# Kernel optimization log

Measured on AMD Instinct MI355X. Metric: run time of the kernel, lower is better.

## Reference

```python
import jax, jax.numpy as jnp
import numpy as np

NUM_USERS = 50000
NUM_ITEMS = 50000
U_IN = 256
I_IN = 256
LATENT = 128
FINAL = 64
NUM_U_GRAPHS = 2
NUM_I_GRAPHS = 2
E = 1000000
BATCH = 16384


def _seg_softmax(scores, seg, n):
    # numerically-stable segment softmax (PyG softmax semantics)
    m = jax.ops.segment_max(scores, seg, num_segments=n)
    e = jnp.exp(scores - m[seg])
    s = jax.ops.segment_sum(e, seg, num_segments=n)
    return e / (s[seg] + 1e-16)


def _gat(S, edges, W1, a_self, a_nb, omega):
    # S: [N, in_dim], edges: [G, 2, E] (row 0 = src j, row 1 = dst i)
    n = S.shape[0]
    H1 = S @ W1                     # [N, latent]
    alpha_self = H1 @ a_self        # [N]
    alpha_nb = H1 @ a_nb            # [N]
    H2 = jnp.zeros_like(H1)
    for g in range(edges.shape[0]):  # small fixed loop over graphs
        src = edges[g, 0]
        dst = edges[g, 1]
        score = jax.nn.leaky_relu(alpha_self[dst] + alpha_nb[src], negative_slope=0.2)
        alpha = _seg_softmax(score, dst, n)                      # [E]
        msg = H1[src] * alpha[:, None]                           # [E, latent]
        H2 = H2 + omega[g] * jax.ops.segment_sum(msg, dst, num_segments=n)
    return H2


def setup_inputs() -> dict:
    key = jax.random.key(0)
    ks = jax.random.split(key, 24)
    d = {}
    d['user_indices'] = jax.random.randint(ks[0], (BATCH,), 0, NUM_USERS)
    d['item_indices'] = jax.random.randint(ks[1], (BATCH,), 0, NUM_ITEMS)
    d['S_u'] = jax.random.normal(ks[2], (NUM_USERS, U_IN), dtype=jnp.float32)
    d['S_b'] = jax.random.normal(ks[3], (NUM_ITEMS, I_IN), dtype=jnp.float32)
    d['edges_u'] = jax.random.randint(ks[4], (NUM_U_GRAPHS, 2, E), 0, NUM_USERS)
    d['edges_b'] = jax.random.randint(ks[5], (NUM_I_GRAPHS, 2, E), 0, NUM_ITEMS)
    s = 0.05
    d['W1_u'] = jax.random.normal(ks[6], (U_IN, LATENT), dtype=jnp.float32) * s
    d['a_self_u'] = jax.random.normal(ks[7], (LATENT,), dtype=jnp.float32) * s
    d['a_nb_u'] = jax.random.normal(ks[8], (LATENT,), dtype=jnp.float32) * s
    d['omega_u'] = jnp.ones((NUM_U_GRAPHS,), dtype=jnp.float32)
    d['W1_b'] = jax.random.normal(ks[9], (I_IN, LATENT), dtype=jnp.float32) * s
    d['a_self_b'] = jax.random.normal(ks[10], (LATENT,), dtype=jnp.float32) * s
    d['a_nb_b'] = jax.random.normal(ks[11], (LATENT,), dtype=jnp.float32) * s
    d['omega_b'] = jnp.ones((NUM_I_GRAPHS,), dtype=jnp.float32)
    d['Wu2'] = jax.random.normal(ks[12], (LATENT, LATENT), dtype=jnp.float32) * s
    d['Wus2_w'] = jax.random.normal(ks[13], (U_IN, LATENT), dtype=jnp.float32) * s
    d['Wus2_b'] = jnp.zeros((LATENT,), dtype=jnp.float32)
    d['Wb2'] = jax.random.normal(ks[14], (LATENT, LATENT), dtype=jnp.float32) * s
    d['Wbs2_w'] = jax.random.normal(ks[15], (I_IN, LATENT), dtype=jnp.float32) * s
    d['Wbs2_b'] = jnp.zeros((LATENT,), dtype=jnp.float32)
    d['Wu3'] = jax.random.normal(ks[16], (LATENT, FINAL), dtype=jnp.float32) * s
    d['Wb3'] = jax.random.normal(ks[17], (LATENT, FINAL), dtype=jnp.float32) * s
    d['Hu4'] = jax.random.normal(ks[18], (NUM_USERS, FINAL), dtype=jnp.float32) * 0.01
    d['Hb4'] = jax.random.normal(ks[19], (NUM_ITEMS, FINAL), dtype=jnp.float32) * 0.01
    d['bu'] = jnp.zeros((NUM_USERS,), dtype=jnp.float32)
    d['bb'] = jnp.zeros((NUM_ITEMS,), dtype=jnp.float32)
    d['bx'] = jnp.zeros((), dtype=jnp.float32)
    return d


def reference(user_indices, item_indices, S_u, S_b, edges_u, edges_b,
              W1_u, a_self_u, a_nb_u, omega_u,
              W1_b, a_self_b, a_nb_b, omega_b,
              Wu2, Wus2_w, Wus2_b, Wb2, Wbs2_w, Wbs2_b,
              Wu3, Wb3, Hu4, Hb4, bu, bb, bx):
    r_min, r_max = 1.0, 5.0
    H_u_2 = _gat(S_u, edges_u, W1_u, a_self_u, a_nb_u, omega_u)
    H_b_2 = _gat(S_b, edges_b, W1_b, a_self_b, a_nb_b, omega_b)
    H_u_3 = jax.nn.elu(H_u_2 @ Wu2 + S_u @ Wus2_w + Wus2_b)
    H_b_3 = jax.nn.elu(H_b_2 @ Wb2 + S_b @ Wbs2_w + Wbs2_b)
    U_all = jax.nn.elu(H_u_3 @ Wu3) + Hu4
    B_all = jax.nn.elu(H_b_3 @ Wb3) + Hb4
    U_batch = U_all[user_indices]
    B_batch = B_all[item_indices]
    dot = jnp.sum(U_batch * B_batch, axis=1)
    raw = dot + bu[user_indices] + bb[item_indices] + bx
    return (r_max - r_min) * jax.nn.sigmoid(raw) + r_min
```

## Files before the change

### kernel.cpp

```cpp
#include <hip/hip_runtime.h>
#include <math.h>

#define N_NODES 50000
#define IN_DIM  256
#define LATENT  128
#define FINALD  64
#define NGRAPH  2
#define NEDGE   1000000
#define BATCHSZ 16384

#define VN4     (4 * N_NODES)
#define NBU     ((VN4 + 255) >> 8)
#define E4      (4 * NEDGE)
#define NPB     256
#define PCH     ((E4 + NPB - 1) / NPB)
#define BCAP    8192
#define PREPB   768

#define WSP_SIDE   98304
#define HSTRIDE    (N_NODES * LATENT)
#define H1STRIDE8  ((size_t)N_NODES * 128)

typedef __attribute__((ext_vector_type(8))) short bf16x8;
typedef __attribute__((ext_vector_type(8))) _Float16 f16x8;
typedef __attribute__((ext_vector_type(4))) float f32x4;
typedef __attribute__((ext_vector_type(2))) float f32x2;
typedef __attribute__((ext_vector_type(8))) unsigned short u16x8;
typedef __attribute__((ext_vector_type(2))) unsigned int u32x2;

__device__ inline unsigned short f2bf(float x) {
    unsigned int u = __float_as_uint(x);
    u = (u + 0x7fffu + ((u >> 16) & 1u)) >> 16;
    return (unsigned short)u;
}
__device__ inline float bf2f(unsigned short h) {
    return __uint_as_float(((unsigned int)h) << 16);
}
__device__ inline unsigned char f2fp8(float x) {
    int p = __builtin_amdgcn_cvt_pk_fp8_f32(x, x, 0, false);
    return (unsigned char)(p & 0xFF);
}

#define BM 128
#define BK 64

__device__ inline int swz(int r, int k) {
    return r * BK + ((((k >> 3) ^ (r & 7)) << 3) | (k & 7));
}
__device__ inline int swz2(int r, int c) {
    return r * 128 + ((((c >> 3) ^ (r & 7)) << 3) | (c & 7));
}

__device__ inline void edge_decomp(int i, int& side, int& g, int& idx) {
    if (i < NEDGE)          { side = 0; g = 0; idx = i; }
    else if (i < 2 * NEDGE) { side = 0; g = 1; idx = i - NEDGE; }
    else if (i < 3 * NEDGE) { side = 1; g = 0; idx = i - 2 * NEDGE; }
    else                    { side = 1; g = 1; idx = i - 3 * NEDGE; }
}

__global__ __launch_bounds__(256)
void fat_count_prep(const int* __restrict__ eU, const int* __restrict__ eB,
                    int* __restrict__ pcnt,
                    const float* __restrict__ W1u, const float* __restrict__ Wu2,
                    const float* __restrict__ Wus2, const float* __restrict__ Wu3,
                    const float* __restrict__ W1b, const float* __restrict__ Wb2,
                    const float* __restrict__ Wbs2, const float* __restrict__ Wb3,
                    unsigned short* __restrict__ dst)
{
    __shared__ int h[NBU];
    int tid = threadIdx.x;
    if (blockIdx.x < NPB) {
        for (int i = tid; i < NBU; i += 256) h[i] = 0;
        __syncthreads();
        int start = blockIdx.x * PCH;
        int stop  = min(start + PCH, E4);
        for (int i = start + tid; i < stop; i += 256) {
            int side, g, idx;
            edge_decomp(i, side, g, idx);
            const int* base = side ? eB : eU;
            int d = base[(size_t)(2 * g + 1) * NEDGE + idx];
            int vd = side * (2 * N_NODES) + g * N_NODES + d;
            atomicAdd(&h[vd >> 8], 1);
        }
        __syncthreads();
        for (int i = tid; i < NBU; i += 256)
            pcnt[i * NPB + blockIdx.x] = h[i];
    } else {
        int e = (blockIdx.x - NPB) * 256 + tid;
        if (e >= 2 * WSP_SIDE) return;
        int side = e >= WSP_SIDE;
        int r = e - (side ? WSP_SIDE : 0);
        const float* src; int K, hoff; int w3 = 0, fp16 = 0;
        if (r < 32768)      { src = side ? W1b  : W1u;  K = 256; hoff = 0;     }
        else if (r < 49152) { src = side ? Wb2  : Wu2;  K = 128; hoff = 32768; r -= 32768; fp16 = 1; }
        else if (r < 81920) { src = side ? Wbs2 : Wus2; K = 256; hoff = 49152; r -= 49152; }
        else                { src = side ? Wb3  : Wu3;  K = 128; hoff = 81920; r -= 81920; w3 = 1; }
        int n = (K == 256) ? (r >> 8) : (r >> 7);
        int k = (K == 256) ? (r & 255) : (r & 127);
        float x;
        if (w3) x = (n < 64) ? src[k * 64 + n] : 0.f;
        else    x = src[k * 128 + n];
        unsigned short o;
        if (fp16) { _Float16 hx = (_Float16)x; o = *(unsigned short*)&hx; }
        else      o = f2bf(x);
        dst[(size_t)side * WSP_SIDE + hoff + n * K + k] = o;
    }
}

__global__ __launch_bounds__(1024)
void part_scan(const int* __restrict__ pcnt, int* __restrict__ pbase,
               int* __restrict__ bbase, int* __restrict__ offs)
{
    __shared__ int btot[NBU];
    __shared__ int wsum2[16];
    int tid = threadIdx.x;
    int lane = tid & 63, w = tid >> 6;
    for (int b = w; b < NBU; b += 16) {
        int4 v = *(const int4*)&pcnt[b * NPB + lane * 4];
        int s = v.x + v.y + v.z + v.w;
        int x = s;
        #pragma unroll
        for (int o = 1; o < 64; o <<= 1) {
            int y = __shfl_up(x, o);
            if (lane >= o) x += y;
        }
        int ex = x - s;
        int* pb = &pbase[b * NPB + lane * 4];
        pb[0] = ex;
        pb[1] = ex + v.x;
        pb[2] = ex + v.x + v.y;
        pb[3] = ex + v.x + v.y + v.z;
        if (lane == 63) btot[b] = x;
    }
    __syncthreads();
    int v = (tid < NBU) ? btot[tid] : 0;
    int x = v;
    #pragma unroll
    for (int o = 1; o < 64; o <<= 1) {
        int y = __shfl_up(x, o);
        if (lane >= o) x += y;
    }
    if (lane == 63) wsum2[w] = x;
    __syncthreads();
    int wb = 0;
    for (int i = 0; i < w; ++i) wb += wsum2[i];
    int ex = wb + x - v;
    if (tid < NBU) bbase[tid] = ex;
    if (tid == NBU - 1) bbase[NBU] = ex + v;
    if (tid == 0) offs[VN4] = E4;
}

__global__ __launch_bounds__(256)
void fat_fill_gemm1(const int* __restrict__ eU, const int* __restrict__ eB,
                    const int* __restrict__ pbase, const int* __restrict__ bbase,
                    int* __restrict__ ebuf,
                    const float* __restrict__ Su, const float* __restrict__ Sb,
                    const unsigned short* __restrict__ wspb,
                    const float* __restrict__ aself_u, const float* __restrict__ anbv_u,
                    const float* __restrict__ aself_b, const float* __restrict__ anbv_b,
                    unsigned char* __restrict__ H1f8, float* __restrict__ asf,
                    float* __restrict__ anb, int M)
{
    __shared__ unsigned short AhS[BM * BK];
    __shared__ unsigned short BhS[BM * BK];
    __shared__ float dotL[BM][2];
    __shared__ int lbase[NBU];
    __shared__ int lcur[NBU];

    int tid = threadIdx.x;

    if (blockIdx.x < NPB) {
        for (int i = tid; i < NBU; i += 256) {
            lbase[i] = bbase[i] + pbase[i * NPB + blockIdx.x];
            lcur[i] = 0;
        }
        __syncthreads();
        int start = blockIdx.x * PCH;
        int stop  = min(start + PCH, E4);
        for (int i = start + tid; i < stop; i += 256) {
            int side, g, idx;
            edge_decomp(i, side, g, idx);
            const int* base = side ? eB : eU;
            int src = base[(size_t)(2 * g) * NEDGE + idx];
            int d = base[(size_t)(2 * g + 1) * NEDGE + idx];
            int vd = side * (2 * N_NODES) + g * N_NODES + d;
            int b = vd >> 8;
            int p = lbase[b] + atomicAdd(&lcur[b], 1);
            ebuf[p] = ((vd & 255) << 16) | src;
        }
        return;
    }

    int t = blockIdx.x - NPB;
    const int side = t / 391;
    const int rowBase = (t % 391) * BM;
    const float* Ap = side ? Sb : Su;
    const unsigned short* Bp = wspb + (size_t)side * WSP_SIDE;
    const float* avs = side ? aself_b : aself_u;
    const float* avn = side ? anbv_b : anbv_u;
    unsigned char* Cout = H1f8 + (size_t)side * H1STRIDE8;

    const int wave = tid >> 6, lane = tid & 63;
    const int wr = wave >> 1, wc = wave & 1;
    const int sl = lane & 15, lg = lane >> 4;
    const int K = IN_DIM;

    if (tid < BM) { dotL[tid][0] = 0.f; dotL[tid][1] = 0.f; }

    f32x4 acc[4][4] = {};

    for (int k0 = 0; k0 < K; k0 += BK) {
        __syncthreads();
        #pragma unroll
        for (int p = 0; p < 4; ++p) {
            int q = p * 256 + tid;
            int row = q >> 3;
            int kq = (q & 7) << 3;
            int grow = rowBase + row;
            u16x8 hv = {0, 0, 0, 0, 0, 0, 0, 0};
            if (grow < M) {
                const float* a = Ap + (size_t)grow * K + k0 + kq;
                float4 v0 = *(const float4*)a;
                float4 v1 = *(const float4*)(a + 4);
                hv[0] = f2bf(v0.x); hv[1] = f2bf(v0.y); hv[2] = f2bf(v0.z); hv[3] = f2bf(v0.w);
                hv[4] = f2bf(v1.x); hv[5] = f2bf(v1.y); hv[6] = f2bf(v1.z); hv[7] = f2bf(v1.w);
            }
            *(u16x8*)&AhS[swz(row, kq)] = hv;
        }
        #pragma unroll
        for (int p = 0; p < 4; ++p) {
            int q = p * 256 + tid;
            int n = q >> 3;
            int kq = (q & 7) << 3;
            u16x8 hv = *(const u16x8*)(Bp + (size_t)n * K + k0 + kq);
            *(u16x8*)&BhS[swz(n, kq)] = hv;
        }
        __syncthreads();
        #pragma unroll
        for (int ks = 0; ks < 2; ++ks) {
            int kof = ks * 32 + lg * 8;
            bf16x8 af[4], bf[4];
            #pragma unroll
            for (int f = 0; f < 4; ++f) {
                af[f] = *(const bf16x8*)&AhS[swz(wr * 64 + f * 16 + sl, kof)];
                bf[f] = *(const bf16x8*)&BhS[swz(wc * 64 + f * 16 + sl, kof)];
            }
            #pragma unroll
            for (int fm = 0; fm < 4; ++fm)
                #pragma unroll
                for (int fn = 0; fn < 4; ++fn)
                    acc[fm][fn] = __builtin_amdgcn_mfma_f32_16x16x32_bf16(af[fm], bf[fn], acc[fm][fn], 0, 0, 0);
        }
    }

    #pragma unroll
    for (int fm = 0; fm < 4; ++fm)
        #pragma unroll
        for (int r = 0; r < 4; ++r) {
            int row = rowBase + wr * 64 + fm * 16 + lg * 4 + r;
            if (row >= M) continue;
            #pragma unroll
            for (int fn = 0; fn < 4; ++fn) {
                int col = wc * 64 + fn * 16 + sl;
                Cout[(size_t)row * 128 + col] = f2fp8(acc[fm][fn][r]);
            }
        }

    float as_[4], an_[4];
    #pragma unroll
    for (int fn = 0; fn < 4; ++fn) {
        int col = wc * 64 + fn * 16 + sl;
        as_[fn] = avs[col];
        an_[fn] = avn[col];
    }
    #pragma unroll
    for (int fm = 0; fm < 4; ++fm)
        #pragma unroll
        for (int r = 0; r < 4; ++r) {
            float p1 = 0.f, p2 = 0.f;
            #pragma unroll
            for (int fn = 0; fn < 4; ++fn) {
                float v = acc[fm][fn][r];
                p1 += v * as_[fn];
                p2 += v * an_[fn];
            }
            #pragma unroll
            for (int o = 1; o <= 8; o <<= 1) {
                p1 += __shfl_xor(p1, o);
                p2 += __shfl_xor(p2, o);
            }
            if (sl == 0) {
                int row_l = wr * 64 + fm * 16 + lg * 4 + r;
                atomicAdd(&dotL[row_l][0], p1);
                atomicAdd(&dotL[row_l][1], p2);
            }
        }
    __syncthreads();
    if (tid < BM) {
        int row = rowBase + tid;
        if (row < M) {
            asf[side * M + row] = dotL[tid][0];
            anb[side * M + row] = dotL[tid][1];
        }
    }
}

__global__ __launch_bounds__(256)
void bucket_csr(const int* __restrict__ ebuf, const int* __restrict__ bbase,
                int* __restrict__ offs, unsigned short* __restrict__ csr)
{
    __shared__ int lds_e[BCAP];
    __shared__ int cnt[256];
    __shared__ int excl[256];
    __shared__ int cur[256];
    __shared__ int wsum[4];
    int tid = threadIdx.x;
    int b = blockIdx.x;
    int lo = bbase[b], hi = bbase[b + 1];
    int sz = hi - lo;

    cnt[tid] = 0; cur[tid] = 0;
    __syncthreads();
    for (int i = tid; i < sz; i += 256) {
        int v = ebuf[lo + i];
        if (i < BCAP) lds_e[i] = v;
        atomicAdd(&cnt[v >> 16], 1);
    }
    __syncthreads();

    int lane = tid & 63, w = tid >> 6;
    int v = cnt[tid];
    int x = v;
    #pragma unroll
    for (int o = 1; o < 64; o <<= 1) {
        int y = __shfl_up(x, o);
        if (lane >= o) x += y;
    }
    if (lane == 63) wsum[w] = x;
    __syncthreads();
    int wb = 0;
    for (int i = 0; i < w; ++i) wb += wsum[i];
    int ex = wb + x - v;
    excl[tid] = ex;
    int vd = b * 256 + tid;
    if (vd < VN4) offs[vd] = lo + ex;
    __syncthreads();

    for (int i = tid; i < sz; i += 256) {
        int e = (i < BCAP) ? lds_e[i] : ebuf[lo + i];
        int dl = e >> 16;
        int p = excl[dl] + atomicAdd(&cur[dl], 1);
        csr[lo + p] = (unsigned short)(e & 0xFFFF);
    }
}

__global__ __launch_bounds__(256)
void gat_gather(const unsigned char* __restrict__ H1f8, const float* __restrict__ asf,
                const float* __restrict__ anb,
                const int* __restrict__ offs, const unsigned short* __restrict__ csr,
                const float* __restrict__ omu, const float* __restrict__ omb,
                unsigned short* __restrict__ H2h, int n)
{
    int side = blockIdx.y;
    int lane = threadIdx.x & 63, wid = threadIdx.x >> 6;
    int d = blockIdx.x * 4 + wid;
    if (d >= n) return;
    const unsigned char* Hbase = H1f8 + (size_t)side * H1STRIDE8;
    const int* offside = offs + side * 2 * N_NODES;
    const float* om_p = side ? omb : omu;
    float ad = asf[side * n + d];
    const float* anb_s = anb + side * n;
    int sub = lane >> 4, sl = lane & 15;
    const unsigned char* Hp = Hbase + (sl << 3);
    float fin[8] = {};

    #pragma unroll
    for (int g = 0; g < NGRAPH; ++g) {
        int beg = offside[g * n + d], end = offside[g * n + d + 1];
        float om = om_p[g];
        float un[8] = {};
        float ss = 0.f;

        int e = beg + sub;
        for (; e + 4 < end; e += 8) {
            int s0 = csr[e], s1 = csr[e + 4];
            float a0 = anb_s[s0], a1 = anb_s[s1];
            u32x2 b0 = *(const u32x2*)(Hp + (size_t)s0 * 128);
            u32x2 b1 = *(const u32x2*)(Hp + (size_t)s1 * 128);
            float sc0 = ad + a0; sc0 = fmaxf(sc0, 0.2f * sc0);
            float sc1 = ad + a1; sc1 = fmaxf(sc1, 0.2f * sc1);
            float w0 = __expf(sc0), w1 = __expf(sc1);
            ss += w0 + w1;
            {
                f32x2 q0 = __builtin_amdgcn_cvt_pk_f32_fp8(b0[0], false);
                f32x2 q1 = __builtin_amdgcn_cvt_pk_f32_fp8(b0[0], true);
                f32x2 q2 = __builtin_amdgcn_cvt_pk_f32_fp8(b0[1], false);
                f32x2 q3 = __builtin_amdgcn_cvt_pk_f32_fp8(b0[1], true);
                un[0] += w0 * q0[0]; un[1] += w0 * q0[1];
                un[2] += w0 * q1[0]; un[3] += w0 * q1[1];
                un[4] += w0 * q2[0]; un[5] += w0 * q2[1];
                un[6] += w0 * q3[0]; un[7] += w0 * q3[1];
            }
            {
                f32x2 q0 = __builtin_amdgcn_cvt_pk_f32_fp8(b1[0], false);
                f32x2 q1 = __builtin_amdgcn_cvt_pk_f32_fp8(b1[0], true);
                f32x2 q2 = __builtin_amdgcn_cvt_pk_f32_fp8(b1[1], false);
                f32x2 q3 = __builtin_amdgcn_cvt_pk_f32_fp8(b1[1], true);
                un[0] += w1 * q0[0]; un[1] += w1 * q0[1];
                un[2] += w1 * q1[0]; un[3] += w1 * q1[1];
                un[4] += w1 * q2[0]; un[5] += w1 * q2[1];
                un[6] += w1 * q3[0]; un[7] += w1 * q3[1];
            }
        }
        if (e < end) {
            int s0 = csr[e];
            float a0 = anb_s[s0];
            u32x2 b0 = *(const u32x2*)(Hp + (size_t)s0 * 128);
            float sc0 = ad + a0; sc0 = fmaxf(sc0, 0.2f * sc0);
            float w0 = __expf(sc0);
            ss += w0;
            f32x2 q0 = __builtin_amdgcn_cvt_pk_f32_fp8(b0[0], false);
            f32x2 q1 = __builtin_amdgcn_cvt_pk_f32_fp8(b0[0], true);
            f32x2 q2 = __builtin_amdgcn_cvt_pk_f32_fp8(b0[1], false);
            f32x2 q3 = __builtin_amdgcn_cvt_pk_f32_fp8(b0[1], true);
            un[0] += w0 * q0[0]; un[1] += w0 * q0[1];
            un[2] += w0 * q1[0]; un[3] += w0 * q1[1];
            un[4] += w0 * q2[0]; un[5] += w0 * q2[1];
            un[6] += w0 * q3[0]; un[7] += w0 * q3[1];
        }

        ss += __shfl_xor(ss, 32);
        ss += __shfl_xor(ss, 16);
        float wsc = om / (ss + 1e-16f);
        #pragma unroll
        for (int j = 0; j < 8; ++j) fin[j] += wsc * un[j];
    }

    #pragma unroll
    for (int j = 0; j < 8; ++j) {
        fin[j] += __shfl_xor(fin[j], 32);
        fin[j] += __shfl_xor(fin[j], 16);
    }
    if (sub == 0) {
        f16x8 o;
        #pragma unroll
        for (int j = 0; j < 8; ++j) o[j] = (_Float16)fin[j];
        *(f16x8*)(H2h + (size_t)side * HSTRIDE + (size_t)d * LATENT + sl * 8) = o;
    }
}

__global__ __launch_bounds__(256)
void gemm_fused23(const unsigned short* __restrict__ H2h,
                  const float* __restrict__ Su, const float* __restrict__ Sb,
                  const unsigned short* __restrict__ wspb,
                  const float* __restrict__ b2u, const float* __restrict__ b2b,
                  const float* __restrict__ H4u, const float* __restrict__ H4b,
                  float* __restrict__ Uo, float* __restrict__ Bo, int M)
{
    __shared__ unsigned short sm[BM * BK * 2];
    __shared__ unsigned short W3S[64 * 128];
    unsigned short* AhS = sm;
    unsigned short* BhS = sm + BM * BK;

    const int side = blockIdx.z;
    const unsigned short* Bside = wspb + (size_t)side * WSP_SIDE;
    const float* bias = side ? b2b : b2u;
    const float* H4 = side ? H4b : H4u;
    float* Cout = side ? Bo : Uo;

    const int tid = threadIdx.x;
    const int rowBase = blockIdx.x * BM;
    const int wave = tid >> 6, lane = tid & 63;
    const int wr = wave >> 1, wc = wave & 1;
    const int sl = lane & 15, lg = lane >> 4;

    {
        const unsigned short* w3 = Bside + 81920;
        #pragma unroll
        for (int p = 0; p < 4; ++p) {
            int i = p * 256 + tid;
            int n = i >> 4;
            int kq = (i & 15) << 3;
            u16x8 v = *(const u16x8*)(w3 + (size_t)n * 128 + kq);
            *(u16x8*)&W3S[swz2(n, kq)] = v;
        }
    }

    f32x4 acc[4][4] = {};

    {
        const unsigned short* Ap = H2h + (size_t)side * HSTRIDE;
        const unsigned short* Bp = Bside + 32768;
        const int K = LATENT;
        for (int k0 = 0; k0 < K; k0 += BK) {
            __syncthreads();
            #pragma unroll
            for (int p = 0; p < 4; ++p) {
                int q = p * 256 + tid;
                int row = q >> 3;
                int kq = (q & 7) << 3;
                int grow = rowBase + row;
                u16x8 hv = {0, 0, 0, 0, 0, 0, 0, 0};
                if (grow < M)
                    hv = *(const u16x8*)(Ap + (size_t)grow * K + k0 + kq);
                *(u16x8*)&AhS[swz(row, kq)] = hv;
            }
            #pragma unroll
            for (int p = 0; p < 4; ++p) {
                int q = p * 256 + tid;
                int n = q >> 3;
                int kq = (q & 7) << 3;
                u16x8 hv = *(const u16x8*)(Bp + (size_t)n * K + k0 + kq);
                *(u16x8*)&BhS[swz(n, kq)] = hv;
            }
            __syncthreads();
            #pragma unroll
            for (int ks = 0; ks < 2; ++ks) {
                int kof = ks * 32 + lg * 8;
                f16x8 af[4], bf[4];
                #pragma unroll
                for (int f = 0; f < 4; ++f) {
                    af[f] = *(const f16x8*)&AhS[swz(wr * 64 + f * 16 + sl, kof)];
                    bf[f] = *(const f16x8*)&BhS[swz(wc * 64 + f * 16 + sl, kof)];
                }
                #pragma unroll
                for (int fm = 0; fm < 4; ++fm)
                    #pragma unroll
                    for (int fn = 0; fn < 4; ++fn)
                        acc[fm][fn] = __builtin_amdgcn_mfma_f32_16x16x32_f16(af[fm], bf[fn], acc[fm][fn], 0, 0, 0);
            }
        }
    }

    {
        const float* Ap = side ? Sb : Su;
        const unsigned short* Bp = Bside + 49152;
        const int K = IN_DIM;
        for (int k0 = 0; k0 < K; k0 += BK) {
            __syncthreads();
            #pragma unroll
            for (int p = 0; p < 4; ++p) {
                int q = p * 256 + tid;
                int row = q >> 3;
                int kq = (q & 7) << 3;
                int grow = rowBase + row;
                u16x8 hv = {0, 0, 0, 0, 0, 0, 0, 0};
                if (grow < M) {
                    const float* a = Ap + (size_t)grow * K + k0 + kq;
                    float4 v0 = *(const float4*)a;
                    float4 v1 = *(const float4*)(a + 4);
                    hv[0] = f2bf(v0.x); hv[1] = f2bf(v0.y); hv[2] = f2bf(v0.z); hv[3] = f2bf(v0.w);
                    hv[4] = f2bf(v1.x); hv[5] = f2bf(v1.y); hv[6] = f2bf(v1.z); hv[7] = f2bf(v1.w);
                }
                *(u16x8*)&AhS[swz(row, kq)] = hv;
            }
            #pragma unroll
            for (int p = 0; p < 4; ++p) {
                int q = p * 256 + tid;
                int n = q >> 3;
                int kq = (q & 7) << 3;
                u16x8 hv = *(const u16x8*)(Bp + (size_t)n * K + k0 + kq);
                *(u16x8*)&BhS[swz(n, kq)] = hv;
            }
            __syncthreads();
            #pragma unroll
            for (int ks = 0; ks < 2; ++ks) {
                int kof = ks * 32 + lg * 8;
                bf16x8 af[4], bf[4];
                #pragma unroll
                for (int f = 0; f < 4; ++f) {
                    af[f] = *(const bf16x8*)&AhS[swz(wr * 64 + f * 16 + sl, kof)];
                    bf[f] = *(const bf16x8*)&BhS[swz(wc * 64 + f * 16 + sl, kof)];
                }
                #pragma unroll
                for (int fm = 0; fm < 4; ++fm)
                    #pragma unroll
                    for (int fn = 0; fn < 4; ++fn)
                        acc[fm][fn] = __builtin_amdgcn_mfma_f32_16x16x32_bf16(af[fm], bf[fn], acc[fm][fn], 0, 0, 0);
            }
        }
    }

    __syncthreads();
    unsigned short* H3S = sm;

    #pragma unroll
    for (int fm = 0; fm < 4; ++fm)
        #pragma unroll
        for (int r = 0; r < 4; ++r) {
            int row_l = wr * 64 + fm * 16 + lg * 4 + r;
            #pragma unroll
            for (int fn = 0; fn < 4; ++fn) {
                int col = wc * 64 + fn * 16 + sl;
                float v = acc[fm][fn][r] + bias[col];
                v = v > 0.f ? v : (__expf(v) - 1.f);
                H3S[swz2(row_l, col)] = f2bf(v);
            }
        }
    __syncthreads();

    f32x4 acc2[4][2] = {};
    #pragma unroll
    for (int ks = 0; ks < 4; ++ks) {
        int kof = ks * 32 + lg * 8;
        bf16x8 a2[4], b2f[2];
        #pragma unroll
        for (int f = 0; f < 4; ++f)
            a2[f] = *(const bf16x8*)&H3S[swz2(wr * 64 + f * 16 + sl, kof)];
        #pragma unroll
        for (int f = 0; f < 2; ++f)
            b2f[f] = *(const bf16x8*)&W3S[swz2(wc * 32 + f * 16 + sl, kof)];
        #pragma unroll
        for (int fm = 0; fm < 4; ++fm)
            #pragma unroll
            for (int fn = 0; fn < 2; ++fn)
                acc2[fm][fn] = __builtin_amdgcn_mfma_f32_16x16x32_bf16(a2[fm], b2f[fn], acc2[fm][fn], 0, 0, 0);
    }

    #pragma unroll
    for (int fm = 0; fm < 4; ++fm)
        #pragma unroll
        for (int r = 0; r < 4; ++r) {
            int row = rowBase + wr * 64 + fm * 16 + lg * 4 + r;
            if (row >= M) continue;
            #pragma unroll
            for (int fn = 0; fn < 2; ++fn) {
                int col = wc * 32 + fn * 16 + sl;
                float v = acc2[fm][fn][r];
                v = v > 0.f ? v : (__expf(v) - 1.f);
                v += H4[(size_t)row * FINALD + col];
                Cout[(size_t)row * FINALD + col] = v;
            }
        }
}

__global__ __launch_bounds__(256)
void predict(const int* __restrict__ uid, const int* __restrict__ iid,
             const float* __restrict__ U, const float* __restrict__ B,
             const float* __restrict__ bu, const float* __restrict__ bb,
             const float* __restrict__ bx, float* __restrict__ out, int batch)
{
    int lane = threadIdx.x & 63, wid = threadIdx.x >> 6;
    int b = blockIdx.x * 4 + wid;
    if (b >= batch) return;
    int u = uid[b], it = iid[b];
    float p = U[(size_t)u * FINALD + lane] * B[(size_t)it * FINALD + lane];
    #pragma unroll
    for (int o = 32; o; o >>= 1) p += __shfl_xor(p, o);
    if (lane == 0) {
        float raw = p + bu[u] + bb[it] + bx[0];
        out[b] = 4.f * (1.f / (1.f + __expf(-raw))) + 1.f;
    }
}

extern "C" void kernel_launch(void* const* d_in, const int* in_sizes, int n_in,
                              void* d_out, int out_size, void* d_ws, size_t ws_size,
                              hipStream_t stream)
{
    const int N = N_NODES;

    float* ws = (float*)d_ws;
    unsigned char* H1f8 = (unsigned char*)ws;
    unsigned short* H2h = (unsigned short*)(ws + 6400000);
    float* U_all = ws + 12800000;
    float* B_all = ws + 16000000;
    float* asf   = ws + 19200000;
    float* anb   = asf + 2 * N;
    int*   offs  = (int*)(anb + 2 * N);
    int*   bbase = offs + VN4 + 1;
    unsigned short* csr = (unsigned short*)(bbase + NBU + 1);
    unsigned short* wsp = (unsigned short*)(((uintptr_t)(csr + E4) + 15) & ~(uintptr_t)15);
    int*   ebuf  = (int*)H2h;
    int*   pcnt  = (int*)U_all;
    int*   pbase = pcnt + NBU * NPB;

    const int* eU = (const int*)d_in[4];
    const int* eB = (const int*)d_in[5];
    const float* Su = (const float*)d_in[2];
    const float* Sb = (const float*)d_in[3];

    fat_count_prep<<<NPB + PREPB, 256, 0, stream>>>(
        eU, eB, pcnt,
        (const float*)d_in[6],  (const float*)d_in[14], (const float*)d_in[15], (const float*)d_in[20],
        (const float*)d_in[10], (const float*)d_in[17], (const float*)d_in[18], (const float*)d_in[21],
        wsp);

    part_scan<<<1, 1024, 0, stream>>>(pcnt, pbase, bbase, offs);

    fat_fill_gemm1<<<NPB + 782, 256, 0, stream>>>(
        eU, eB, pbase, bbase, ebuf,
        Su, Sb, wsp,
        (const float*)d_in[7], (const float*)d_in[8],
        (const float*)d_in[11], (const float*)d_in[12],
        H1f8, asf, anb, N);

    bucket_csr<<<NBU, 256, 0, stream>>>(ebuf, bbase, offs, csr);

    gat_gather<<<dim3(N / 4, 2), 256, 0, stream>>>(
        H1f8, asf, anb, offs, csr,
        (const float*)d_in[9], (const float*)d_in[13], H2h, N);

    gemm_fused23<<<dim3(391, 1, 2), 256, 0, stream>>>(
        H2h, Su, Sb, wsp,
        (const float*)d_in[16], (const float*)d_in[19],
        (const float*)d_in[22], (const float*)d_in[23],
        U_all, B_all, N);

    predict<<<BATCHSZ / 4, 256, 0, stream>>>(
        (const int*)d_in[0], (const int*)d_in[1], U_all, B_all,
        (const float*)d_in[24], (const float*)d_in[25], (const float*)d_in[26],
        (float*)d_out, BATCHSZ);
}
```

Baseline: 288.9 us.

## Precompute edge attention weights in CSR build and pack with source index

The CSR construction kernel now computes each edge's leaky-relu score and exponential (via exp2 with log2e pre-scaled attention dots) and stores it as fp16 packed alongside the 16-bit source index in a 32-bit entry. The gather kernel then reads the weight directly instead of doing a random load of the neighbour attention value and an exp per edge. This trades a doubled CSR size and fp16 rounding of unnormalised weights (overflow risk without max subtraction) for fewer dependent random loads in the gather. The random anb load moves into the bucket kernel instead.

```diff
diff --git a/kernel.cpp b/kernel.cpp
--- a/kernel.cpp
+++ b/kernel.cpp
@@ -28,6 +28,14 @@
 typedef __attribute__((ext_vector_type(8))) unsigned short u16x8;
 typedef __attribute__((ext_vector_type(2))) unsigned int u32x2;
 
+#if __has_builtin(__builtin_amdgcn_exp2f)
+#define LOGSCALE 1.44269504f
+#define EXPW(x)  __builtin_amdgcn_exp2f(x)
+#else
+#define LOGSCALE 1.0f
+#define EXPW(x)  __expf(x)
+#endif
+
 __device__ inline unsigned short f2bf(float x) {
     unsigned int u = __float_as_uint(x);
     u = (u + 0x7fffu + ((u >> 16) & 1u)) >> 16;
@@ -39,6 +47,14 @@
 __device__ inline unsigned char f2fp8(float x) {
     int p = __builtin_amdgcn_cvt_pk_fp8_f32(x, x, 0, false);
     return (unsigned char)(p & 0xFF);
+}
+__device__ inline unsigned short f2f16bits(float x) {
+    _Float16 h = (_Float16)x;
+    return *(unsigned short*)&h;
+}
+__device__ inline float f16bits2f(unsigned short h) {
+    _Float16 x = *(_Float16*)&h;
+    return (float)x;
 }
 
 #define BM 128
@@ -101,7 +117,7 @@
         if (w3) x = (n < 64) ? src[k * 64 + n] : 0.f;
         else    x = src[k * 128 + n];
         unsigned short o;
-        if (fp16) { _Float16 hx = (_Float16)x; o = *(unsigned short*)&hx; }
+        if (fp16) o = f2f16bits(x);
         else      o = f2bf(x);
         dst[(size_t)side * WSP_SIDE + hoff + n * K + k] = o;
     }
@@ -299,15 +315,16 @@
     if (tid < BM) {
         int row = rowBase + tid;
         if (row < M) {
-            asf[side * M + row] = dotL[tid][0];
-            anb[side * M + row] = dotL[tid][1];
+            asf[side * M + row] = dotL[tid][0] * LOGSCALE;
+            anb[side * M + row] = dotL[tid][1] * LOGSCALE;
         }
     }
 }
 
 __global__ __launch_bounds__(256)
 void bucket_csr(const int* __restrict__ ebuf, const int* __restrict__ bbase,
-                int* __restrict__ offs, unsigned short* __restrict__ csr)
+                int* __restrict__ offs, unsigned int* __restrict__ csrw,
+                const float* __restrict__ asf, const float* __restrict__ anb)
 {
     __shared__ int lds_e[BCAP];
     __shared__ int cnt[256];
@@ -342,22 +359,30 @@
     for (int i = 0; i < w; ++i) wb += wsum[i];
     int ex = wb + x - v;
     excl[tid] = ex;
-    int vd = b * 256 + tid;
-    if (vd < VN4) offs[vd] = lo + ex;
+    int vd0 = b * 256 + tid;
+    if (vd0 < VN4) offs[vd0] = lo + ex;
     __syncthreads();
 
     for (int i = tid; i < sz; i += 256) {
         int e = (i < BCAP) ? lds_e[i] : ebuf[lo + i];
         int dl = e >> 16;
+        int src = e & 0xFFFF;
         int p = excl[dl] + atomicAdd(&cur[dl], 1);
-        csr[lo + p] = (unsigned short)(e & 0xFFFF);
+        int vd = b * 256 + dl;
+        int side = vd >= 2 * N_NODES;
+        int rem = vd - side * 2 * N_NODES;
+        int g = rem >= N_NODES;
+        int dd = rem - g * N_NODES;
+        float sc = asf[side * N_NODES + dd] + anb[side * N_NODES + src];
+        sc = fmaxf(sc, 0.2f * sc);
+        float wv = EXPW(sc);
+        csrw[lo + p] = ((unsigned int)f2f16bits(wv) << 16) | (unsigned int)src;
     }
 }
 
 __global__ __launch_bounds__(256)
-void gat_gather(const unsigned char* __restrict__ H1f8, const float* __restrict__ asf,
-                const float* __restrict__ anb,
-                const int* __restrict__ offs, const unsigned short* __restrict__ csr,
+void gat_gather(const unsigned char* __restrict__ H1f8,
+                const int* __restrict__ offs, const unsigned int* __restrict__ csrw,
                 const float* __restrict__ omu, const float* __restrict__ omb,
                 unsigned short* __restrict__ H2h, int n)
 {
@@ -368,8 +393,6 @@
     const unsigned char* Hbase = H1f8 + (size_t)side * H1STRIDE8;
     const int* offside = offs + side * 2 * N_NODES;
     const float* om_p = side ? omb : omu;
-    float ad = asf[side * n + d];
-    const float* anb_s = anb + side * n;
     int sub = lane >> 4, sl = lane & 15;
     const unsigned char* Hp = Hbase + (sl << 3);
     float fin[8] = {};
@@ -383,13 +406,12 @@
 
         int e = beg + sub;
         for (; e + 4 < end; e += 8) {
-            int s0 = csr[e], s1 = csr[e + 4];
-            float a0 = anb_s[s0], a1 = anb_s[s1];
+            unsigned int v0 = csrw[e], v1 = csrw[e + 4];
+            int s0 = v0 & 0xFFFF, s1 = v1 & 0xFFFF;
             u32x2 b0 = *(const u32x2*)(Hp + (size_t)s0 * 128);
             u32x2 b1 = *(const u32x2*)(Hp + (size_t)s1 * 128);
-            float sc0 = ad + a0; sc0 = fmaxf(sc0, 0.2f * sc0);
-            float sc1 = ad + a1; sc1 = fmaxf(sc1, 0.2f * sc1);
-            float w0 = __expf(sc0), w1 = __expf(sc1);
+            float w0 = f16bits2f((unsigned short)(v0 >> 16));
+            float w1 = f16bits2f((unsigned short)(v1 >> 16));
             ss += w0 + w1;
             {
                 f32x2 q0 = __builtin_amdgcn_cvt_pk_f32_fp8(b0[0], false);
@@ -413,11 +435,10 @@
             }
         }
         if (e < end) {
-            int s0 = csr[e];
-            float a0 = anb_s[s0];
+            unsigned int v0 = csrw[e];
+            int s0 = v0 & 0xFFFF;
             u32x2 b0 = *(const u32x2*)(Hp + (size_t)s0 * 128);
-            float sc0 = ad + a0; sc0 = fmaxf(sc0, 0.2f * sc0);
-            float w0 = __expf(sc0);
+            float w0 = f16bits2f((unsigned short)(v0 >> 16));
             ss += w0;
             f32x2 q0 = __builtin_amdgcn_cvt_pk_f32_fp8(b0[0], false);
             f32x2 q1 = __builtin_amdgcn_cvt_pk_f32_fp8(b0[0], true);
@@ -668,8 +689,8 @@
     float* anb   = asf + 2 * N;
     int*   offs  = (int*)(anb + 2 * N);
     int*   bbase = offs + VN4 + 1;
-    unsigned short* csr = (unsigned short*)(bbase + NBU + 1);
-    unsigned short* wsp = (unsigned short*)(((uintptr_t)(csr + E4) + 15) & ~(uintptr_t)15);
+    unsigned int* csrw = (unsigned int*)(bbase + NBU + 1);
+    unsigned short* wsp = (unsigned short*)(csrw + E4);
     int*   ebuf  = (int*)H2h;
     int*   pcnt  = (int*)U_all;
     int*   pbase = pcnt + NBU * NPB;
@@ -694,10 +715,10 @@
         (const float*)d_in[11], (const float*)d_in[12],
         H1f8, asf, anb, N);
 
-    bucket_csr<<<NBU, 256, 0, stream>>>(ebuf, bbase, offs, csr);
+    bucket_csr<<<NBU, 256, 0, stream>>>(ebuf, bbase, offs, csrw, asf, anb);
 
     gat_gather<<<dim3(N / 4, 2), 256, 0, stream>>>(
-        H1f8, asf, anb, offs, csr,
+        H1f8, offs, csrw,
         (const float*)d_in[9], (const float*)d_in[13], H2h, N);
 
     gemm_fused23<<<dim3(391, 1, 2), 256, 0, stream>>>(
```

Measured after the change: 298.7 us. 1.03x slower.
